# Performance work log

Hardware: AMD Instinct MI355X
Metric: run time of the kernel (lower is better)

The kernel has to match this reference:

```python
import jax, jax.numpy as jnp
import numpy as np

BN_EPS = 1e-5
NUM_SUBSET = 3


def setup_inputs() -> dict:
    key = jax.random.key(0)
    ks = jax.random.split(key, 6)
    N, C, T, V = 64, 192, 128, 25
    return {
        "x": jax.random.normal(ks[0], (N, C, T, V), dtype=jnp.float32),
        "Wqkv": jax.random.normal(ks[1], (3 * C, C), dtype=jnp.float32) * 0.05,
        "bqkv": jax.random.normal(ks[2], (3 * C,), dtype=jnp.float32) * 0.05,
        "Wff": jax.random.normal(ks[3], (C, C), dtype=jnp.float32) * 0.05,
        "bff": jax.random.normal(ks[4], (C,), dtype=jnp.float32) * 0.05,
        "gamma": jnp.ones((C,), dtype=jnp.float32),
        "beta": jnp.zeros((C,), dtype=jnp.float32),
        "running_mean": jnp.zeros((C,), dtype=jnp.float32),
        "running_var": jax.random.uniform(ks[5], (C,), dtype=jnp.float32) + 0.5,
    }


def reference(x, Wqkv, bqkv, Wff, bff, gamma, beta, running_mean, running_var):
    N, C, T, V = x.shape
    S = NUM_SUBSET
    mid = C // S  # mid_dim
    # 1x1 conv C -> 3C, then view (N, 3S, mid, T, V) and chunk into q,k,v
    qkv = jnp.einsum('nctv,oc->notv', x, Wqkv) + bqkv[None, :, None, None]
    qkv = qkv.reshape(N, 3 * S, mid, T, V)
    q, k, v = jnp.split(qkv, 3, axis=1)  # each (N, S, mid, T, V)
    # joint attention over V: contract channel and time, tanh instead of softmax
    att = jnp.tanh(jnp.einsum('nsctu,nsctv->nsuv', q, k) / (mid * T))  # (N,S,V,V)
    # weighted aggregation back to (N, C, T, V)
    y = jnp.einsum('nsuv,nsctv->nsctu', att, v).reshape(N, C, T, V)
    # ff_nets: 1x1 conv + BatchNorm2d (eval mode, running stats)
    y = jnp.einsum('nctv,oc->notv', y, Wff) + bff[None, :, None, None]
    inv = gamma / jnp.sqrt(running_var + BN_EPS)
    y = y * inv[None, :, None, None] + (beta - running_mean * inv)[None, :, None, None]
    # residual + LeakyReLU(0.1)
    out = jax.nn.leaky_relu(x + y, negative_slope=0.1)
    return (out, att)
```

## Files before the change

### kernel.cpp

```cpp
#include <hip/hip_runtime.h>
#include <hip/hip_bf16.h>

typedef __attribute__((ext_vector_type(8))) short bf16x8;
typedef __attribute__((ext_vector_type(4))) float f32x4;

#define MFMA16(a, b, c) __builtin_amdgcn_mfma_f32_16x16x32_bf16((a), (b), (c), 0, 0, 0)

#define N_ 64
#define C_ 192
#define T_ 128
#define V_ 25
#define S_ 3
#define MID 64
#define TV 3200
#define C3 576
#define OUT_ELEMS 39321600ULL
#define NCHUNK 16
#define PSTRIDE 640

static __device__ __forceinline__ float bf2f(ushort u) {
    union { unsigned int i; float f; } x; x.i = ((unsigned int)u) << 16; return x.f;
}
static __device__ __forceinline__ ushort f2bf(float f) {
    union { float f; unsigned int i; } x; x.f = f;
    unsigned int r = x.i + 0x7fffu + ((x.i >> 16) & 1u);
    return (ushort)(r >> 16);
}
static __device__ __forceinline__ unsigned int pack2(float a, float b) {
    return (unsigned int)f2bf(a) | ((unsigned int)f2bf(b) << 16);
}

__global__ __launch_bounds__(256) void k1_qkv(const float* __restrict__ x,
                                              const float* __restrict__ W,
                                              const float* __restrict__ bias,
                                              ushort* __restrict__ qkvT) {
    int m0 = blockIdx.x * 64, n = blockIdx.y;
    __shared__ ushort As[64 * 200];
    __shared__ ushort Bs[64 * 200];
    __shared__ float biasS[64];
    unsigned int* scratchU = (unsigned int*)Bs;
    ushort* scratchS = Bs;
    int tid = threadIdx.x;

    for (int cg = 0; cg < 2; cg++) {
        if (cg) __syncthreads();
#pragma unroll
        for (int j = 0; j < 6; j++) {
            int chunk = tid + j * 256;
            int cc = chunk >> 4, m4 = chunk & 15;
            float4 d = *(const float4*)(x + ((size_t)n * C_ + cg * 96 + cc) * TV + m0 + m4 * 4);
            scratchU[cc * 35 + m4 * 2]     = pack2(d.x, d.y);
            scratchU[cc * 35 + m4 * 2 + 1] = pack2(d.z, d.w);
        }
        __syncthreads();
#pragma unroll
        for (int j = 0; j < 24; j++) {
            int idx = tid + j * 256;
            int mm = idx / 96, cc = idx % 96;
            As[mm * 200 + cg * 96 + cc] = scratchS[cc * 70 + mm];
        }
    }

    int wave = tid >> 6, lane = tid & 63;
    int mb = (wave >> 1) * 32, ob = (wave & 1) * 32;
    int lrow = lane & 15, lk = lane >> 4;

    for (int oi = 0; oi < 9; oi++) {
        int o0 = oi * 64;
        __syncthreads();
#pragma unroll
        for (int j = 0; j < 12; j++) {
            int chunk = tid + j * 256;
            int r = chunk / 48, c4 = chunk % 48;
            float4 d = *(const float4*)(W + (size_t)(o0 + r) * C_ + c4 * 4);
            ushort* dst = &Bs[r * 200 + c4 * 4];
            dst[0] = f2bf(d.x); dst[1] = f2bf(d.y); dst[2] = f2bf(d.z); dst[3] = f2bf(d.w);
        }
        if (tid < 64) biasS[tid] = bias[o0 + tid];
        __syncthreads();

        f32x4 acc[2][2];
#pragma unroll
        for (int i = 0; i < 2; i++)
#pragma unroll
            for (int j = 0; j < 2; j++) acc[i][j] = (f32x4){0.f, 0.f, 0.f, 0.f};

#pragma unroll
        for (int ks = 0; ks < 6; ks++) {
            bf16x8 a[2], b[2];
#pragma unroll
            for (int mt = 0; mt < 2; mt++)
                a[mt] = *(const bf16x8*)&As[(mb + mt * 16 + lrow) * 200 + ks * 32 + lk * 8];
#pragma unroll
            for (int ot = 0; ot < 2; ot++)
                b[ot] = *(const bf16x8*)&Bs[(ob + ot * 16 + lrow) * 200 + ks * 32 + lk * 8];
#pragma unroll
            for (int mt = 0; mt < 2; mt++)
#pragma unroll
                for (int ot = 0; ot < 2; ot++)
                    acc[mt][ot] = MFMA16(a[mt], b[ot], acc[mt][ot]);
        }

        ushort* op = qkvT + ((size_t)n * TV + m0) * C3 + o0;
#pragma unroll
        for (int mt = 0; mt < 2; mt++) {
#pragma unroll
            for (int ot = 0; ot < 2; ot++) {
                int o = ob + ot * 16 + lrow;
                float bv = biasS[o];
#pragma unroll
                for (int r = 0; r < 4; r++) {
                    int m = mb + mt * 16 + lk * 4 + r;
                    op[(size_t)m * C3 + o] = f2bf(acc[mt][ot][r] + bv);
                }
            }
        }
    }
}

__global__ __launch_bounds__(256) void k2_att(const ushort* __restrict__ qkvT,
                                              float* __restrict__ partial) {
    int tc = blockIdx.x, s = blockIdx.y, n = blockIdx.z;
    __shared__ ushort tiles[4 * 2 * 32 * 72];
    __shared__ float red[4 * 32 * 33];
    int tid = threadIdx.x, wave = tid >> 6, lane = tid & 63;
    ushort* myQ = &tiles[wave * 2 * 2304];
    ushort* myK = myQ + 2304;

    if (lane < 63) {
        *(uint4*)&myQ[1800 + lane * 8] = (uint4){0, 0, 0, 0};
        *(uint4*)&myK[1800 + lane * 8] = (uint4){0, 0, 0, 0};
    }

    const size_t nbase = (size_t)n * TV * C3;
    int qoff = s * MID;
    int koff = C_ + s * MID;
    int lrow = lane & 15, lk = lane >> 4;

    f32x4 acc[2][2];
#pragma unroll
    for (int i = 0; i < 2; i++)
#pragma unroll
        for (int j = 0; j < 2; j++) acc[i][j] = (f32x4){0.f, 0.f, 0.f, 0.f};

#pragma unroll
    for (int i = 0; i < 2; i++) {
        int t = tc * 8 + wave + 4 * i;
#pragma unroll
        for (int j = 0; j < 7; j++) {
            int idx = lane + j * 64;
            if (idx < 400) {
                int op = idx / 200, rr = idx % 200;
                int row = rr >> 3, c16 = rr & 7;
                int chan = (op ? koff : qoff) + c16 * 8;
                uint4 d = *(const uint4*)(qkvT + nbase + (size_t)(t * V_ + row) * C3 + chan);
                *(uint4*)((op ? myK : myQ) + row * 72 + c16 * 8) = d;
            }
        }
#pragma unroll
        for (int ks = 0; ks < 2; ks++) {
            bf16x8 a0 = *(const bf16x8*)&myQ[lrow * 72 + ks * 32 + lk * 8];
            bf16x8 a1 = *(const bf16x8*)&myQ[(16 + lrow) * 72 + ks * 32 + lk * 8];
            bf16x8 b0 = *(const bf16x8*)&myK[lrow * 72 + ks * 32 + lk * 8];
            bf16x8 b1 = *(const bf16x8*)&myK[(16 + lrow) * 72 + ks * 32 + lk * 8];
            acc[0][0] = MFMA16(a0, b0, acc[0][0]);
            acc[0][1] = MFMA16(a0, b1, acc[0][1]);
            acc[1][0] = MFMA16(a1, b0, acc[1][0]);
            acc[1][1] = MFMA16(a1, b1, acc[1][1]);
        }
    }

#pragma unroll
    for (int ub = 0; ub < 2; ub++)
#pragma unroll
        for (int vb = 0; vb < 2; vb++)
#pragma unroll
            for (int r = 0; r < 4; r++) {
                int u = ub * 16 + lk * 4 + r, v = vb * 16 + lrow;
                red[wave * 1056 + u * 33 + v] = acc[ub][vb][r];
            }
    __syncthreads();

    float* pb = partial + (((size_t)n * S_ + s) * NCHUNK + tc) * PSTRIDE;
    for (int idx = tid; idx < 1024; idx += 256) {
        int u = idx >> 5, v = idx & 31;
        if (u < V_ && v < V_) {
            float sum = red[u * 33 + v] + red[1056 + u * 33 + v] +
                        red[2112 + u * 33 + v] + red[3168 + u * 33 + v];
            pb[u * V_ + v] = sum;
        }
    }
}

__global__ __launch_bounds__(256) void k2_reduce(const float* __restrict__ partial,
                                                 float* __restrict__ attOut) {
    int idx = blockIdx.x * 256 + threadIdx.x;
    if (idx >= 192 * 625) return;
    int ns = idx / 625, r = idx % 625;
    const float* p = partial + (size_t)ns * NCHUNK * PSTRIDE + r;
    float s = 0.f;
#pragma unroll
    for (int j = 0; j < NCHUNK; j++) s += p[j * PSTRIDE];
    attOut[(size_t)ns * 625 + r] = tanhf(s * (1.0f / 8192.0f));
}

__global__ __launch_bounds__(192) void k3_y(const ushort* __restrict__ qkvT,
                                            const float* __restrict__ attF,
                                            ushort* __restrict__ yT) {
    int t = blockIdx.x, n = blockIdx.y;
    __shared__ float attS[3 * 700];
    int tid = threadIdx.x;
    const float* ab = attF + (size_t)n * (S_ * V_ * V_);
    for (int idx = tid; idx < S_ * V_ * V_; idx += 192) {
        int s = idx / 625, r = idx % 625;
        attS[s * 700 + (r / 25) * 28 + (r % 25)] = ab[idx];
    }
    __syncthreads();

    int c = tid;
    int s = c >> 6;
    const ushort* vb = qkvT + ((size_t)n * TV + (size_t)t * V_) * C3 + 2 * C_ + c;
    float vreg[25];
#pragma unroll
    for (int v = 0; v < 25; v++) vreg[v] = bf2f(vb[(size_t)v * C3]);

    ushort* yb = yT + ((size_t)n * TV + (size_t)t * V_) * C_ + c;
    const float* as = &attS[s * 700];
    for (int u = 0; u < 25; u++) {
        float a = 0.f;
#pragma unroll
        for (int v = 0; v < 25; v++) a += as[u * 28 + v] * vreg[v];
        yb[(size_t)u * C_] = f2bf(a);
    }
}

__global__ __launch_bounds__(256) void k4_out(const ushort* __restrict__ yT,
                                              const float* __restrict__ Wff,
                                              const float* __restrict__ bff,
                                              const float* __restrict__ gamma,
                                              const float* __restrict__ beta,
                                              const float* __restrict__ rmean,
                                              const float* __restrict__ rvar,
                                              const float* __restrict__ x,
                                              float* __restrict__ out) {
    int m0 = blockIdx.x * 64, n = blockIdx.y;
    __shared__ ushort As[64 * 200];
    __shared__ ushort Bs[64 * 200];
    __shared__ float invS[64], shiftS[64];
    float* zT = (float*)Bs;
    int tid = threadIdx.x;

    const ushort* ab = yT + ((size_t)n * TV + m0) * C_;
#pragma unroll
    for (int j = 0; j < 6; j++) {
        int chunk = tid + j * 256;
        int r = chunk / 24, c16 = chunk % 24;
        *(uint4*)&As[r * 200 + c16 * 8] = *(const uint4*)(ab + (size_t)r * C_ + c16 * 8);
    }

    int wave = tid >> 6, lane = tid & 63;
    int mb = (wave >> 1) * 32, obw = (wave & 1) * 32;
    int lrow = lane & 15, lk = lane >> 4;

    for (int oi = 0; oi < 3; oi++) {
        int o0 = oi * 64;
        __syncthreads();
#pragma unroll
        for (int j = 0; j < 12; j++) {
            int chunk = tid + j * 256;
            int r = chunk / 48, c4 = chunk % 48;
            float4 d = *(const float4*)(Wff + (size_t)(o0 + r) * C_ + c4 * 4);
            ushort* dst = &Bs[r * 200 + c4 * 4];
            dst[0] = f2bf(d.x); dst[1] = f2bf(d.y); dst[2] = f2bf(d.z); dst[3] = f2bf(d.w);
        }
        if (tid < 64) {
            int o = o0 + tid;
            float inv = gamma[o] * rsqrtf(rvar[o] + 1e-5f);
            invS[tid] = inv;
            shiftS[tid] = beta[o] - rmean[o] * inv + bff[o] * inv;
        }
        __syncthreads();

        f32x4 acc[2][2];
#pragma unroll
        for (int i = 0; i < 2; i++)
#pragma unroll
            for (int j = 0; j < 2; j++) acc[i][j] = (f32x4){0.f, 0.f, 0.f, 0.f};

#pragma unroll
        for (int ks = 0; ks < 6; ks++) {
            bf16x8 a[2], b[2];
#pragma unroll
            for (int mt = 0; mt < 2; mt++)
                a[mt] = *(const bf16x8*)&As[(mb + mt * 16 + lrow) * 200 + ks * 32 + lk * 8];
#pragma unroll
            for (int ot = 0; ot < 2; ot++)
                b[ot] = *(const bf16x8*)&Bs[(obw + ot * 16 + lrow) * 200 + ks * 32 + lk * 8];
#pragma unroll
            for (int mt = 0; mt < 2; mt++)
#pragma unroll
                for (int ot = 0; ot < 2; ot++)
                    acc[mt][ot] = MFMA16(a[mt], b[ot], acc[mt][ot]);
        }

        __syncthreads();
#pragma unroll
        for (int mt = 0; mt < 2; mt++)
#pragma unroll
            for (int ot = 0; ot < 2; ot++) {
                int o = obw + ot * 16 + lrow;
                float inv = invS[o], sh = shiftS[o];
#pragma unroll
                for (int r = 0; r < 4; r++) {
                    int m = mb + mt * 16 + lk * 4 + r;
                    zT[o * 68 + m] = acc[mt][ot][r] * inv + sh;
                }
            }
        __syncthreads();

        const float* xb = x + ((size_t)n * C_ + o0) * TV + m0;
        float* ob2 = out + ((size_t)n * C_ + o0) * TV + m0;
#pragma unroll
        for (int j = 0; j < 4; j++) {
            int chunk = tid + j * 256;
            int o = chunk >> 4, m4 = chunk & 15;
            float4 zv = *(float4*)&zT[o * 68 + m4 * 4];
            float4 xv = *(const float4*)(xb + (size_t)o * TV + m4 * 4);
            float4 res; float a;
            a = xv.x + zv.x; res.x = (a >= 0.f) ? a : 0.1f * a;
            a = xv.y + zv.y; res.y = (a >= 0.f) ? a : 0.1f * a;
            a = xv.z + zv.z; res.z = (a >= 0.f) ? a : 0.1f * a;
            a = xv.w + zv.w; res.w = (a >= 0.f) ? a : 0.1f * a;
            *(float4*)(ob2 + (size_t)o * TV + m4 * 4) = res;
        }
    }
}

extern "C" void kernel_launch(void* const* d_in, const int* in_sizes, int n_in,
                              void* d_out, int out_size, void* d_ws, size_t ws_size,
                              hipStream_t stream) {
    (void)in_sizes; (void)n_in; (void)out_size; (void)ws_size;
    const float* x    = (const float*)d_in[0];
    const float* Wqkv = (const float*)d_in[1];
    const float* bqkv = (const float*)d_in[2];
    const float* Wff  = (const float*)d_in[3];
    const float* bff  = (const float*)d_in[4];
    const float* gam  = (const float*)d_in[5];
    const float* bet  = (const float*)d_in[6];
    const float* rme  = (const float*)d_in[7];
    const float* rva  = (const float*)d_in[8];
    float* out = (float*)d_out;
    float* attOut = out + OUT_ELEMS;

    char* ws = (char*)d_ws;
    ushort* qkvT = (ushort*)ws;
    float*  partial = (float*)(ws + 235929600);
    ushort* yT      = (ushort*)(ws + 235929600);

    k1_qkv<<<dim3(50, 64), 256, 0, stream>>>(x, Wqkv, bqkv, qkvT);
    k2_att<<<dim3(NCHUNK, 3, 64), 256, 0, stream>>>(qkvT, partial);
    k2_reduce<<<dim3(469), 256, 0, stream>>>(partial, attOut);
    k3_y<<<dim3(128, 64), 192, 0, stream>>>(qkvT, attOut, yT);
    k4_out<<<dim3(50, 64), 256, 0, stream>>>(yT, Wff, bff, gam, bet, rme, rva, x, out);
}
```

Measured before the change: 514.7 us.

## Pre-convert weights to bf16 once and read MFMA B operands from global

Adds a small conversion kernel that turns Wqkv and Wff into bf16 buffers in the workspace ahead of the GEMM kernels. The GEMM kernels then load B fragments straight from those global bf16 weights instead of converting them into shared memory on every output tile. This removes per-block conversion work and per-tile barriers and shrinks LDS use, so more blocks can be resident (launch bounds now request 4 per SM for k1). Bias and BN constants are also staged once per block. The cost is two extra launches and uncoalesced, cache-dependent global fragment loads in the inner loop. Workspace regions are reused (WffB overwrites the start of qkvT after k3), which relies on stream ordering.

```diff
diff --git a/kernel.cpp b/kernel.cpp
--- a/kernel.cpp
+++ b/kernel.cpp
@@ -30,55 +30,57 @@
     return (unsigned int)f2bf(a) | ((unsigned int)f2bf(b) << 16);
 }
 
-__global__ __launch_bounds__(256) void k1_qkv(const float* __restrict__ x,
-                                              const float* __restrict__ W,
-                                              const float* __restrict__ bias,
-                                              ushort* __restrict__ qkvT) {
+__global__ __launch_bounds__(256) void kconv(const float* __restrict__ src,
+                                             ushort* __restrict__ dst, int n4) {
+    int i = blockIdx.x * 256 + threadIdx.x;
+    if (i < n4) {
+        float4 d = *(const float4*)(src + (size_t)i * 4);
+        unsigned int* o = (unsigned int*)dst + (size_t)i * 2;
+        o[0] = pack2(d.x, d.y);
+        o[1] = pack2(d.z, d.w);
+    }
+}
+
+__global__ __launch_bounds__(256, 4) void k1_qkv(const float* __restrict__ x,
+                                                 const ushort* __restrict__ Wbf,
+                                                 const float* __restrict__ bias,
+                                                 ushort* __restrict__ qkvT) {
     int m0 = blockIdx.x * 64, n = blockIdx.y;
     __shared__ ushort As[64 * 200];
-    __shared__ ushort Bs[64 * 200];
-    __shared__ float biasS[64];
-    unsigned int* scratchU = (unsigned int*)Bs;
-    ushort* scratchS = Bs;
+    __shared__ unsigned int scratchU[64 * 35];
+    __shared__ float biasS[C3];
+    ushort* scratchS = (ushort*)scratchU;
     int tid = threadIdx.x;
 
-    for (int cg = 0; cg < 2; cg++) {
+    for (int i = tid; i < C3; i += 256) biasS[i] = bias[i];
+
+    for (int cg = 0; cg < 3; cg++) {
         if (cg) __syncthreads();
 #pragma unroll
-        for (int j = 0; j < 6; j++) {
+        for (int j = 0; j < 4; j++) {
             int chunk = tid + j * 256;
             int cc = chunk >> 4, m4 = chunk & 15;
-            float4 d = *(const float4*)(x + ((size_t)n * C_ + cg * 96 + cc) * TV + m0 + m4 * 4);
+            float4 d = *(const float4*)(x + ((size_t)n * C_ + cg * 64 + cc) * TV + m0 + m4 * 4);
             scratchU[cc * 35 + m4 * 2]     = pack2(d.x, d.y);
             scratchU[cc * 35 + m4 * 2 + 1] = pack2(d.z, d.w);
         }
         __syncthreads();
 #pragma unroll
-        for (int j = 0; j < 24; j++) {
+        for (int j = 0; j < 16; j++) {
             int idx = tid + j * 256;
-            int mm = idx / 96, cc = idx % 96;
-            As[mm * 200 + cg * 96 + cc] = scratchS[cc * 70 + mm];
-        }
-    }
+            int mm = idx >> 6, cc = idx & 63;
+            As[mm * 200 + cg * 64 + cc] = scratchS[cc * 70 + mm];
+        }
+    }
+    __syncthreads();
 
     int wave = tid >> 6, lane = tid & 63;
     int mb = (wave >> 1) * 32, ob = (wave & 1) * 32;
     int lrow = lane & 15, lk = lane >> 4;
 
+#pragma unroll 1
     for (int oi = 0; oi < 9; oi++) {
         int o0 = oi * 64;
-        __syncthreads();
-#pragma unroll
-        for (int j = 0; j < 12; j++) {
-            int chunk = tid + j * 256;
-            int r = chunk / 48, c4 = chunk % 48;
-            float4 d = *(const float4*)(W + (size_t)(o0 + r) * C_ + c4 * 4);
-            ushort* dst = &Bs[r * 200 + c4 * 4];
-            dst[0] = f2bf(d.x); dst[1] = f2bf(d.y); dst[2] = f2bf(d.z); dst[3] = f2bf(d.w);
-        }
-        if (tid < 64) biasS[tid] = bias[o0 + tid];
-        __syncthreads();
-
         f32x4 acc[2][2];
 #pragma unroll
         for (int i = 0; i < 2; i++)
@@ -93,7 +95,7 @@
                 a[mt] = *(const bf16x8*)&As[(mb + mt * 16 + lrow) * 200 + ks * 32 + lk * 8];
 #pragma unroll
             for (int ot = 0; ot < 2; ot++)
-                b[ot] = *(const bf16x8*)&Bs[(ob + ot * 16 + lrow) * 200 + ks * 32 + lk * 8];
+                b[ot] = *(const bf16x8*)&Wbf[(size_t)(o0 + ob + ot * 16 + lrow) * C_ + ks * 32 + lk * 8];
 #pragma unroll
             for (int mt = 0; mt < 2; mt++)
 #pragma unroll
@@ -107,7 +109,7 @@
 #pragma unroll
             for (int ot = 0; ot < 2; ot++) {
                 int o = ob + ot * 16 + lrow;
-                float bv = biasS[o];
+                float bv = biasS[o0 + o];
 #pragma unroll
                 for (int r = 0; r < 4; r++) {
                     int m = mb + mt * 16 + lk * 4 + r;
@@ -235,7 +237,7 @@
 }
 
 __global__ __launch_bounds__(256) void k4_out(const ushort* __restrict__ yT,
-                                              const float* __restrict__ Wff,
+                                              const ushort* __restrict__ Wbf,
                                               const float* __restrict__ bff,
                                               const float* __restrict__ gamma,
                                               const float* __restrict__ beta,
@@ -245,42 +247,31 @@
                                               float* __restrict__ out) {
     int m0 = blockIdx.x * 64, n = blockIdx.y;
     __shared__ ushort As[64 * 200];
-    __shared__ ushort Bs[64 * 200];
-    __shared__ float invS[64], shiftS[64];
-    float* zT = (float*)Bs;
+    __shared__ float zT[64 * 68];
+    __shared__ float invS[C_], shiftS[C_];
     int tid = threadIdx.x;
 
     const ushort* ab = yT + ((size_t)n * TV + m0) * C_;
 #pragma unroll
     for (int j = 0; j < 6; j++) {
         int chunk = tid + j * 256;
-        int r = chunk / 24, c16 = chunk % 24;
-        *(uint4*)&As[r * 200 + c16 * 8] = *(const uint4*)(ab + (size_t)r * C_ + c16 * 8);
-    }
+        int r = chunk / 24, c8 = chunk % 24;
+        *(uint4*)&As[r * 200 + c8 * 8] = *(const uint4*)(ab + (size_t)r * C_ + c8 * 8);
+    }
+    if (tid < C_) {
+        float inv = gamma[tid] * rsqrtf(rvar[tid] + 1e-5f);
+        invS[tid] = inv;
+        shiftS[tid] = beta[tid] - rmean[tid] * inv + bff[tid] * inv;
+    }
+    __syncthreads();
 
     int wave = tid >> 6, lane = tid & 63;
     int mb = (wave >> 1) * 32, obw = (wave & 1) * 32;
     int lrow = lane & 15, lk = lane >> 4;
 
+#pragma unroll 1
     for (int oi = 0; oi < 3; oi++) {
         int o0 = oi * 64;
-        __syncthreads();
-#pragma unroll
-        for (int j = 0; j < 12; j++) {
-            int chunk = tid + j * 256;
-            int r = chunk / 48, c4 = chunk % 48;
-            float4 d = *(const float4*)(Wff + (size_t)(o0 + r) * C_ + c4 * 4);
-            ushort* dst = &Bs[r * 200 + c4 * 4];
-            dst[0] = f2bf(d.x); dst[1] = f2bf(d.y); dst[2] = f2bf(d.z); dst[3] = f2bf(d.w);
-        }
-        if (tid < 64) {
-            int o = o0 + tid;
-            float inv = gamma[o] * rsqrtf(rvar[o] + 1e-5f);
-            invS[tid] = inv;
-            shiftS[tid] = beta[o] - rmean[o] * inv + bff[o] * inv;
-        }
-        __syncthreads();
-
         f32x4 acc[2][2];
 #pragma unroll
         for (int i = 0; i < 2; i++)
@@ -295,7 +286,7 @@
                 a[mt] = *(const bf16x8*)&As[(mb + mt * 16 + lrow) * 200 + ks * 32 + lk * 8];
 #pragma unroll
             for (int ot = 0; ot < 2; ot++)
-                b[ot] = *(const bf16x8*)&Bs[(obw + ot * 16 + lrow) * 200 + ks * 32 + lk * 8];
+                b[ot] = *(const bf16x8*)&Wbf[(size_t)(o0 + obw + ot * 16 + lrow) * C_ + ks * 32 + lk * 8];
 #pragma unroll
             for (int mt = 0; mt < 2; mt++)
 #pragma unroll
@@ -309,7 +300,7 @@
 #pragma unroll
             for (int ot = 0; ot < 2; ot++) {
                 int o = obw + ot * 16 + lrow;
-                float inv = invS[o], sh = shiftS[o];
+                float inv = invS[o0 + o], sh = shiftS[o0 + o];
 #pragma unroll
                 for (int r = 0; r < 4; r++) {
                     int m = mb + mt * 16 + lk * 4 + r;
@@ -356,10 +347,14 @@
     ushort* qkvT = (ushort*)ws;
     float*  partial = (float*)(ws + 235929600);
     ushort* yT      = (ushort*)(ws + 235929600);
-
-    k1_qkv<<<dim3(50, 64), 256, 0, stream>>>(x, Wqkv, bqkv, qkvT);
+    ushort* WqkvB   = (ushort*)(ws + 235929600);
+    ushort* WffB    = (ushort*)ws;
+
+    kconv<<<dim3(108), 256, 0, stream>>>(Wqkv, WqkvB, 27648);
+    k1_qkv<<<dim3(50, 64), 256, 0, stream>>>(x, WqkvB, bqkv, qkvT);
     k2_att<<<dim3(NCHUNK, 3, 64), 256, 0, stream>>>(qkvT, partial);
     k2_reduce<<<dim3(469), 256, 0, stream>>>(partial, attOut);
     k3_y<<<dim3(128, 64), 192, 0, stream>>>(qkvT, attOut, yT);
-    k4_out<<<dim3(50, 64), 256, 0, stream>>>(yT, Wff, bff, gam, bet, rme, rva, x, out);
-}
+    kconv<<<dim3(36), 256, 0, stream>>>(Wff, WffB, 9216);
+    k4_out<<<dim3(50, 64), 256, 0, stream>>>(yT, WffB, bff, gam, bet, rme, rva, x, out);
+}
```

Result: slower. 608.9 us (+18.3%).
